# Optimization experiments

Measured on AMD Instinct MI355X. Metric: run time of the kernel, lower is better.

## Reference

```python
import jax, jax.numpy as jnp
import numpy as np

B, N, D = 1, 4301, 768          # batch, tokens (4200 patch + 1 cls + 100 det), dim
H, HD = 12, 64                  # heads, head_dim (all_head_dim = 768)
NDET = 100                      # det tokens at the end of the sequence
EPS = 1e-5                      # torch LayerNorm default eps
SCALE = HD ** -0.5


def setup_inputs() -> dict:
    key = jax.random.key(0)
    ks = jax.random.split(key, 10)
    w = lambda k: jax.random.normal(k, (D, D), dtype=jnp.float32) * 0.02
    return {
        "x": jax.random.normal(ks[0], (B, N, D), dtype=jnp.float32),
        "wq_p": w(ks[1]), "wk_p": w(ks[2]), "wv_p": w(ks[3]),
        "wq_d": w(ks[4]), "wk_d": w(ks[5]), "wv_d": w(ks[6]),
        "bq_p": jnp.zeros((D,), jnp.float32), "bv_p": jnp.zeros((D,), jnp.float32),
        "bq_d": jnp.zeros((D,), jnp.float32), "bv_d": jnp.zeros((D,), jnp.float32),
        "ln_g": jnp.ones((D,), jnp.float32), "ln_b": jnp.zeros((D,), jnp.float32),
        "wo_p": w(ks[7]), "bo_p": jnp.zeros((D,), jnp.float32),
        "wo_d": w(ks[8]), "bo_d": jnp.zeros((D,), jnp.float32),
    }


def reference(x, wq_p, wk_p, wv_p, wq_d, wk_d, wv_d,
              bq_p, bv_p, bq_d, bv_d, ln_g, ln_b,
              wo_p, bo_p, wo_d, bo_d):
    xp = x[:, :-NDET, :]                       # [B, N-100, D] patch (+cls) tokens
    xd = x[:, -NDET:, :]                       # [B, 100, D]   det tokens
    # separate patch/det QKV projections (subln=True path; k has no bias)
    q = jnp.concatenate([xp @ wq_p.T + bq_p, xd @ wq_d.T + bq_d], axis=1)
    k = jnp.concatenate([xp @ wk_p.T,        xd @ wk_d.T],        axis=1)
    v = jnp.concatenate([xp @ wv_p.T + bv_p, xd @ wv_d.T + bv_d], axis=1)
    split = lambda t: t.reshape(B, N, H, HD).transpose(0, 2, 1, 3)  # [B,H,N,HD]
    q, k, v = split(q) * SCALE, split(k), split(v)
    # unfused attention (memory_efficient_attention_pytorch, attn_mask=None)
    attn = jax.nn.softmax(jnp.einsum("bhqd,bhkd->bhqk", q, k), axis=-1)
    o = jnp.einsum("bhqk,bhkd->bhqd", attn, v)
    o = o.transpose(0, 2, 1, 3).reshape(B, N, D)
    # inner_attn_ln (LayerNorm over all_head_dim)
    mu = o.mean(-1, keepdims=True)
    var = ((o - mu) ** 2).mean(-1, keepdims=True)
    o = (o - mu) * jax.lax.rsqrt(var + EPS) * ln_g + ln_b
    # separate patch/det output projections
    out = jnp.concatenate([o[:, :-NDET, :] @ wo_p.T + bo_p,
                           o[:, -NDET:, :] @ wo_d.T + bo_d], axis=1)
    return out
```

## Files before the change

### kernel.cpp

```cpp
#include <hip/hip_runtime.h>
#include <hip/hip_bf16.h>

#define NT 4301
#define NP 4201
#define NDET 100
#define DMODEL 768
#define NHEAD 12
#define HD 64
#define LN_EPS 1e-5f
#define LOG2E 1.4426950408889634f
#define QSCALE (0.125f * LOG2E)
#define NTP 4352
#define NCHUNK 68
#define FRAGSZ 512
#define CHUNKSZ 4096

typedef __hip_bfloat16 bf16;
typedef __attribute__((ext_vector_type(4))) float f32x4;
typedef __attribute__((ext_vector_type(8))) short frag8;

__global__ __launch_bounds__(256) void cast_all_kernel(
    const float* __restrict__ x,
    const float* __restrict__ w0, const float* __restrict__ w1,
    const float* __restrict__ w2, const float* __restrict__ w3,
    const float* __restrict__ w4, const float* __restrict__ w5,
    const float* __restrict__ w6, const float* __restrict__ w7,
    bf16* __restrict__ dst, int nx, int nw, int total) {
    int i4 = (blockIdx.x * 256 + threadIdx.x) * 4;
    if (i4 >= total) return;
    const float* s;
    int off;
    if (i4 < nx) {
        s = x; off = i4;
    } else {
        int r = i4 - nx;
        int w = r / nw;
        off = r - w * nw;
        s = w0;
        if (w == 1) s = w1; else if (w == 2) s = w2; else if (w == 3) s = w3;
        else if (w == 4) s = w4; else if (w == 5) s = w5;
        else if (w == 6) s = w6; else if (w == 7) s = w7;
    }
    float4 v = *(const float4*)(s + off);
    bf16 o[4] = {__float2bfloat16(v.x), __float2bfloat16(v.y),
                 __float2bfloat16(v.z), __float2bfloat16(v.w)};
    *(ushort4*)(dst + i4) = *(ushort4*)o;
}

__global__ __launch_bounds__(256, 4) void qkv_kernel(
    const bf16* __restrict__ xb, const bf16* __restrict__ wbase,
    const float* __restrict__ bq_p, const float* __restrict__ bq_d,
    const float* __restrict__ bv_p, const float* __restrict__ bv_d,
    bf16* __restrict__ Qb, bf16* __restrict__ Ksw, bf16* __restrict__ Vsw) {
    __shared__ bf16 As[64][32];
    __shared__ bf16 Bs[192][32];

    const int tid = threadIdx.x;
    const int wave = tid >> 6, lane = tid & 63;
    const int quad = lane >> 4, l16 = lane & 15;
    const int bx = blockIdx.x;
    const int h = blockIdx.y;
    const int is_det = bx >= 66;
    const int row0 = is_det ? NP + (bx - 66) * 64 : bx * 64;
    const int Mlim = is_det ? NT : NP;
    const int col0 = h * 64;
    const size_t nw = (size_t)DMODEL * DMODEL;
    const bf16* W = wbase + (is_det ? 3 * nw : 0);

    const f32x4 z4 = {0.f, 0.f, 0.f, 0.f};
    f32x4 acc[4][3];
#pragma unroll
    for (int r4 = 0; r4 < 4; ++r4)
#pragma unroll
        for (int f = 0; f < 3; ++f) acc[r4][f] = z4;

    const int srow = tid >> 2;
    const int scol8 = (tid & 3) * 8;
    int a_r = row0 + srow;
    if (a_r >= Mlim) a_r = Mlim - 1;
    const bf16* ap = xb + (size_t)a_r * DMODEL + scol8;
    const bf16* bp = W + (size_t)(col0 + srow) * DMODEL + scol8;

    uint4 areg  = *(const uint4*)(ap);
    uint4 breg0 = *(const uint4*)(bp);
    uint4 breg1 = *(const uint4*)(bp + nw);
    uint4 breg2 = *(const uint4*)(bp + 2 * nw);

    for (int k0 = 0; k0 < DMODEL; k0 += 32) {
        __syncthreads();
        *(uint4*)(&As[srow][scol8]) = areg;
        *(uint4*)(&Bs[srow][scol8]) = breg0;
        *(uint4*)(&Bs[64 + srow][scol8]) = breg1;
        *(uint4*)(&Bs[128 + srow][scol8]) = breg2;
        if (k0 + 32 < DMODEL) {
            areg  = *(const uint4*)(ap + k0 + 32);
            breg0 = *(const uint4*)(bp + k0 + 32);
            breg1 = *(const uint4*)(bp + nw + k0 + 32);
            breg2 = *(const uint4*)(bp + 2 * nw + k0 + 32);
        }
        __asm__ volatile("s_waitcnt lgkmcnt(0)" ::: "memory");
        __builtin_amdgcn_s_barrier();
        __asm__ volatile("" ::: "memory");
        frag8 af[4], bfr[3];
#pragma unroll
        for (int r4 = 0; r4 < 4; ++r4)
            af[r4] = *(const frag8*)(&As[r4 * 16 + l16][quad * 8]);
#pragma unroll
        for (int f = 0; f < 3; ++f)
            bfr[f] = *(const frag8*)(&Bs[wave * 48 + f * 16 + l16][quad * 8]);
#pragma unroll
        for (int r4 = 0; r4 < 4; ++r4)
#pragma unroll
            for (int f = 0; f < 3; ++f)
                acc[r4][f] = __builtin_amdgcn_mfma_f32_16x16x32_bf16(af[r4], bfr[f], acc[r4][f], 0, 0, 0);
        __asm__ volatile("" ::: "memory");
    }

#pragma unroll
    for (int f = 0; f < 3; ++f) {
        const int oc = 3 * wave + f;
        const int opi = oc >> 2;
        const int cin = (oc & 3) * 16 + l16;
        const int c = col0 + cin;
        float bv = 0.f, scale = 1.f;
        if (opi == 0) { bv = (is_det ? bq_d : bq_p)[c]; scale = QSCALE; }
        else if (opi == 2) { bv = (is_det ? bv_d : bv_p)[c]; }
#pragma unroll
        for (int r4 = 0; r4 < 4; ++r4) {
#pragma unroll
            for (int j = 0; j < 4; ++j) {
                const int r = row0 + r4 * 16 + quad * 4 + j;
                if (r >= Mlim) continue;
                const bf16 val = __float2bfloat16((acc[r4][f][j] + bv) * scale);
                if (opi == 0) {
                    Qb[(size_t)r * DMODEL + c] = val;
                } else if (opi == 1) {
                    const int cc = r >> 6, tf = (r >> 4) & 3, ln = r & 15;
                    const int s = cin >> 5, qd = (cin >> 3) & 3, je = cin & 7;
                    Ksw[((size_t)(h * NCHUNK + cc) * 8 + tf * 2 + s) * FRAGSZ +
                        (qd * 16 + ln) * 8 + je] = val;
                } else {
                    const int t = cin >> 4, le = cin & 15;
                    const int cc = r >> 6, rr = r & 63;
                    const int sv = rr >> 5, qv = (rr >> 3) & 3, je = rr & 7;
                    Vsw[((size_t)(h * NCHUNK + cc) * 8 + t * 2 + sv) * FRAGSZ +
                        (qv * 16 + le) * 8 + je] = val;
                }
            }
        }
    }
}

__global__ __launch_bounds__(256, 2) void attn_kernel(
    const bf16* __restrict__ Q, const bf16* __restrict__ Ksw,
    const bf16* __restrict__ Vsw, float* __restrict__ O_part,
    float* __restrict__ l_part, int cpb) {
    __shared__ unsigned short Ps[4][32][72];

    const int tid = threadIdx.x;
    const int wave = tid >> 6, lane = tid & 63;
    const int quad = lane >> 4, l16 = lane & 15;
    const int h = blockIdx.y;
    const int z = blockIdx.z;
    const int qbase = blockIdx.x * 128;
    const int hoff = h * HD;
    const int c0 = z * cpb, c1 = c0 + cpb;

    frag8 ones;
#pragma unroll
    for (int j = 0; j < 8; ++j) ones[j] = (short)0x3F80;

    frag8 qf[2][2];
#pragma unroll
    for (int g = 0; g < 2; ++g) {
        int qr = qbase + wave * 32 + g * 16 + l16;
        if (qr >= NT) qr = NT - 1;
#pragma unroll
        for (int s = 0; s < 2; ++s)
            qf[g][s] = *(const frag8*)(Q + (size_t)qr * DMODEL + hoff + s * 32 + quad * 8);
    }

    const bf16* kb0 = Ksw + (size_t)h * NCHUNK * CHUNKSZ + lane * 8;
    const bf16* vb0 = Vsw + (size_t)h * NCHUNK * CHUNKSZ + lane * 8;

    const f32x4 z4 = {0.f, 0.f, 0.f, 0.f};
    f32x4 accO[2][4], accL[2];
#pragma unroll
    for (int g = 0; g < 2; ++g) {
        accL[g] = z4;
#pragma unroll
        for (int t = 0; t < 4; ++t) accO[g][t] = z4;
    }

    for (int c = c0; c < c1; ++c) {
        const bf16* kc = kb0 + (size_t)c * CHUNKSZ;
        const bf16* vc = vb0 + (size_t)c * CHUNKSZ;
        frag8 kf[8], vf[8];
#pragma unroll
        for (int f = 0; f < 8; ++f) {
            kf[f] = *(const frag8*)(kc + f * FRAGSZ);
            vf[f] = *(const frag8*)(vc + f * FRAGSZ);
        }

        f32x4 S[2][4];
#pragma unroll
        for (int g = 0; g < 2; ++g)
#pragma unroll
            for (int t = 0; t < 4; ++t) {
                f32x4 s0 = __builtin_amdgcn_mfma_f32_16x16x32_bf16(qf[g][0], kf[t * 2 + 0], z4, 0, 0, 0);
                S[g][t]  = __builtin_amdgcn_mfma_f32_16x16x32_bf16(qf[g][1], kf[t * 2 + 1], s0, 0, 0, 0);
            }
        if (c == NCHUNK - 1) {
            const int kbase = c * 64;
#pragma unroll
            for (int t = 0; t < 4; ++t)
                if (kbase + t * 16 + l16 >= NT)
#pragma unroll
                    for (int g = 0; g < 2; ++g)
                        S[g][t][0] = S[g][t][1] = S[g][t][2] = S[g][t][3] = -1e30f;
        }
#pragma unroll
        for (int g = 0; g < 2; ++g)
#pragma unroll
            for (int t = 0; t < 4; ++t)
#pragma unroll
                for (int j = 0; j < 4; j += 2) {
                    float2 f2 = make_float2(__builtin_exp2f(S[g][t][j]),
                                            __builtin_exp2f(S[g][t][j + 1]));
                    __hip_bfloat162 b2 = __float22bfloat162_rn(f2);
                    unsigned int u = *(unsigned int*)&b2;
                    Ps[wave][g * 16 + quad * 4 + j][t * 16 + l16] = (unsigned short)u;
                    Ps[wave][g * 16 + quad * 4 + j + 1][t * 16 + l16] = (unsigned short)(u >> 16);
                }
        __asm__ volatile("" ::: "memory");
#pragma unroll
        for (int s = 0; s < 2; ++s)
#pragma unroll
            for (int g = 0; g < 2; ++g) {
                frag8 pf = *(const frag8*)(&Ps[wave][g * 16 + l16][s * 32 + quad * 8]);
                accL[g] = __builtin_amdgcn_mfma_f32_16x16x32_bf16(pf, ones, accL[g], 0, 0, 0);
#pragma unroll
                for (int t = 0; t < 4; ++t)
                    accO[g][t] = __builtin_amdgcn_mfma_f32_16x16x32_bf16(pf, vf[t * 2 + s], accO[g][t], 0, 0, 0);
            }
        __asm__ volatile("" ::: "memory");
    }

    float* Op = O_part + (size_t)z * NT * DMODEL;
#pragma unroll
    for (int g = 0; g < 2; ++g)
#pragma unroll
        for (int j = 0; j < 4; ++j) {
            const int r = qbase + wave * 32 + g * 16 + quad * 4 + j;
            if (r < NT) {
#pragma unroll
                for (int t = 0; t < 4; ++t)
                    Op[(size_t)r * DMODEL + hoff + t * 16 + l16] = accO[g][t][j];
                if (l16 == 0)
                    l_part[((size_t)z * NHEAD + h) * NTP + r] = accL[g][j];
            }
        }
}

__global__ __launch_bounds__(192) void reduce_ln_kernel(
    const float* __restrict__ O_part, const float* __restrict__ l_part,
    const float* __restrict__ g, const float* __restrict__ b,
    bf16* __restrict__ out, int nsplit) {
    const int n = blockIdx.x;
    const int tid = threadIdx.x;
    const int d0 = tid * 4;
    const int hh = d0 >> 6;

    float4 o = make_float4(0.f, 0.f, 0.f, 0.f);
    float lv = 0.f;
    for (int s = 0; s < nsplit; ++s) {
        float4 v = *(const float4*)(O_part + ((size_t)s * NT + n) * DMODEL + d0);
        o.x += v.x; o.y += v.y; o.z += v.z; o.w += v.w;
        lv += l_part[((size_t)s * NHEAD + hh) * NTP + n];
    }
    const float inv_l = 1.0f / lv;
    float vals[4] = {o.x * inv_l, o.y * inv_l, o.z * inv_l, o.w * inv_l};

    float s = vals[0] + vals[1] + vals[2] + vals[3];
    float s2 = vals[0] * vals[0] + vals[1] * vals[1] + vals[2] * vals[2] + vals[3] * vals[3];
#pragma unroll
    for (int off = 1; off < 64; off <<= 1) {
        s += __shfl_xor(s, off);
        s2 += __shfl_xor(s2, off);
    }
    __shared__ float ss[3], ss2[3];
    const int wave = tid >> 6, lane = tid & 63;
    if (lane == 0) { ss[wave] = s; ss2[wave] = s2; }
    __syncthreads();
    s = ss[0] + ss[1] + ss[2];
    s2 = ss2[0] + ss2[1] + ss2[2];
    const float mu = s * (1.0f / 768.0f);
    float var = s2 * (1.0f / 768.0f) - mu * mu;
    const float inv = rsqrtf(var + LN_EPS);

    unsigned short pk[4];
#pragma unroll
    for (int i = 0; i < 4; ++i) {
        const int d = d0 + i;
        const float v = (vals[i] - mu) * inv * g[d] + b[d];
        bf16 bb = __float2bfloat16(v);
        pk[i] = *(unsigned short*)&bb;
    }
    *(ushort4*)(out + (size_t)n * DMODEL + d0) = *(ushort4*)pk;
}

__global__ __launch_bounds__(256, 2) void out_kernel(
    const bf16* __restrict__ Lb, const bf16* __restrict__ wo,
    const float* __restrict__ bo_p, const float* __restrict__ bo_d,
    float* __restrict__ out) {
    __shared__ bf16 As[128][32];
    __shared__ bf16 Bs[64][32];

    const int tid = threadIdx.x;
    const int wave = tid >> 6, lane = tid & 63;
    const int quad = lane >> 4, l16 = lane & 15;
    const int bx = blockIdx.x;
    const int is_det = bx >= 33;
    const int row0 = is_det ? NP : bx * 128;
    const int Mlim = is_det ? NT : NP;
    const int col0 = blockIdx.y * 64;
    const size_t nw = (size_t)DMODEL * DMODEL;
    const bf16* B = wo + (is_det ? nw : 0);
    const float* bias = is_det ? bo_d : bo_p;

    const f32x4 z4 = {0.f, 0.f, 0.f, 0.f};
    f32x4 acc[2][4];
#pragma unroll
    for (int gg = 0; gg < 2; ++gg)
#pragma unroll
        for (int t = 0; t < 4; ++t) acc[gg][t] = z4;

    const int arow = tid >> 1;
    const int acol = (tid & 1) * 16;
    int a_r = row0 + arow;
    if (a_r >= Mlim) a_r = Mlim - 1;
    const bf16* ap = Lb + (size_t)a_r * DMODEL + acol;
    const int brow = tid >> 2;
    const int bcol = (tid & 3) * 8;
    const bf16* bp = B + (size_t)(col0 + brow) * DMODEL + bcol;

    uint4 areg0 = *(const uint4*)(ap);
    uint4 areg1 = *(const uint4*)(ap + 8);
    uint4 breg  = *(const uint4*)(bp);

    for (int k0 = 0; k0 < DMODEL; k0 += 32) {
        __syncthreads();
        *(uint4*)(&As[arow][acol]) = areg0;
        *(uint4*)(&As[arow][acol + 8]) = areg1;
        *(uint4*)(&Bs[brow][bcol]) = breg;
        if (k0 + 32 < DMODEL) {
            areg0 = *(const uint4*)(ap + k0 + 32);
            areg1 = *(const uint4*)(ap + k0 + 40);
            breg  = *(const uint4*)(bp + k0 + 32);
        }
        __asm__ volatile("s_waitcnt lgkmcnt(0)" ::: "memory");
        __builtin_amdgcn_s_barrier();
        __asm__ volatile("" ::: "memory");
        frag8 af[2], bfq[4];
#pragma unroll
        for (int gg = 0; gg < 2; ++gg)
            af[gg] = *(const frag8*)(&As[wave * 32 + gg * 16 + l16][quad * 8]);
#pragma unroll
        for (int t = 0; t < 4; ++t)
            bfq[t] = *(const frag8*)(&Bs[t * 16 + l16][quad * 8]);
#pragma unroll
        for (int gg = 0; gg < 2; ++gg)
#pragma unroll
            for (int t = 0; t < 4; ++t)
                acc[gg][t] = __builtin_amdgcn_mfma_f32_16x16x32_bf16(af[gg], bfq[t], acc[gg][t], 0, 0, 0);
        __asm__ volatile("" ::: "memory");
    }

#pragma unroll
    for (int gg = 0; gg < 2; ++gg) {
        const int rbase = row0 + wave * 32 + gg * 16 + quad * 4;
#pragma unroll
        for (int t = 0; t < 4; ++t) {
            const int c = col0 + t * 16 + l16;
            const float bv = bias[c];
#pragma unroll
            for (int j = 0; j < 4; ++j) {
                const int r = rbase + j;
                if (r < Mlim) out[(size_t)r * DMODEL + c] = acc[gg][t][j] + bv;
            }
        }
    }
}

extern "C" void kernel_launch(void* const* d_in, const int* in_sizes, int n_in,
                              void* d_out, int out_size, void* d_ws, size_t ws_size,
                              hipStream_t stream) {
    const float* x    = (const float*)d_in[0];
    const float* wq_p = (const float*)d_in[1];
    const float* wk_p = (const float*)d_in[2];
    const float* wv_p = (const float*)d_in[3];
    const float* wq_d = (const float*)d_in[4];
    const float* wk_d = (const float*)d_in[5];
    const float* wv_d = (const float*)d_in[6];
    const float* bq_p = (const float*)d_in[7];
    const float* bv_p = (const float*)d_in[8];
    const float* bq_d = (const float*)d_in[9];
    const float* bv_d = (const float*)d_in[10];
    const float* ln_g = (const float*)d_in[11];
    const float* ln_b = (const float*)d_in[12];
    const float* wo_p = (const float*)d_in[13];
    const float* bo_p = (const float*)d_in[14];
    const float* wo_d = (const float*)d_in[15];
    const float* bo_d = (const float*)d_in[16];
    float* out = (float*)d_out;

    const size_t nx  = (size_t)NT * DMODEL;
    const size_t nsw = (size_t)NHEAD * NCHUNK * CHUNKSZ;
    const size_t nw  = (size_t)DMODEL * DMODEL;

    char* ws = (char*)d_ws;
    bf16* xb   = (bf16*)ws; ws += nx * 2;
    bf16* wqkv = (bf16*)ws; ws += 6 * nw * 2;
    bf16* wob  = (bf16*)ws; ws += 2 * nw * 2;
    bf16* Qb   = (bf16*)ws; ws += nx * 2;
    bf16* Ksw  = (bf16*)ws; ws += nsw * 2;
    bf16* Vsw  = (bf16*)ws; ws += nsw * 2;
    const size_t fixed = (size_t)(ws - (char*)d_ws);

    const size_t per_split = nx * 4 + (size_t)NHEAD * NTP * 4;
    int nsplit = 1;
    if (ws_size >= fixed + 4 * per_split) nsplit = 4;
    else if (ws_size >= fixed + 2 * per_split) nsplit = 2;
    const int cpb = NCHUNK / nsplit;

    float* O_part = (float*)ws;
    float* l_part = (float*)(ws + (size_t)nsplit * nx * 4);
    bf16* Lb = xb;

    const int total = (int)(nx + 8 * nw);
    cast_all_kernel<<<dim3((total / 4 + 255) / 256), dim3(256), 0, stream>>>(
        x, wq_p, wk_p, wv_p, wq_d, wk_d, wv_d, wo_p, wo_d, xb, (int)nx, (int)nw, total);

    qkv_kernel<<<dim3(68, 12), dim3(256), 0, stream>>>(
        xb, wqkv, bq_p, bq_d, bv_p, bv_d, Qb, Ksw, Vsw);

    attn_kernel<<<dim3(34, NHEAD, nsplit), dim3(256), 0, stream>>>(
        Qb, Ksw, Vsw, O_part, l_part, cpb);

    reduce_ln_kernel<<<dim3(NT), dim3(192), 0, stream>>>(
        O_part, l_part, ln_g, ln_b, Lb, nsplit);

    out_kernel<<<dim3(34, 12), dim3(256), 0, stream>>>(Lb, wob, bo_p, bo_d, out);
}
```

Before: 263.6 us.

## Replace LDS round-trip for P fragments with permlane swaps in attention

Computes S transposed (K as the A operand) so each lane holds key-contiguous scores. The bf16 P fragments for the PV MFMA are then assembled in registers with v_permlane32/16_swap instead of being written to and read back from shared memory. This removes the LDS buffer, its stores and loads, and the associated waits per chunk. The tail mask is rewritten for the new per-lane key layout. It relies on the permlane swap instructions and on the register layout matching the MFMA operand layout exactly.

```diff
diff --git a/kernel.cpp b/kernel.cpp
--- a/kernel.cpp
+++ b/kernel.cpp
@@ -18,6 +18,24 @@
 typedef __hip_bfloat16 bf16;
 typedef __attribute__((ext_vector_type(4))) float f32x4;
 typedef __attribute__((ext_vector_type(8))) short frag8;
+typedef __attribute__((ext_vector_type(2))) unsigned int u32x2;
+
+static __device__ __forceinline__ void permlane32_swap(unsigned& a, unsigned& b) {
+#if __has_builtin(__builtin_amdgcn_permlane32_swap)
+    u32x2 r = __builtin_amdgcn_permlane32_swap(a, b, false, false);
+    a = r[0]; b = r[1];
+#else
+    asm("v_permlane32_swap_b32 %0, %1" : "+v"(a), "+v"(b));
+#endif
+}
+static __device__ __forceinline__ void permlane16_swap(unsigned& a, unsigned& b) {
+#if __has_builtin(__builtin_amdgcn_permlane16_swap)
+    u32x2 r = __builtin_amdgcn_permlane16_swap(a, b, false, false);
+    a = r[0]; b = r[1];
+#else
+    asm("v_permlane16_swap_b32 %0, %1" : "+v"(a), "+v"(b));
+#endif
+}
 
 __global__ __launch_bounds__(256) void cast_all_kernel(
     const float* __restrict__ x,
@@ -155,8 +173,6 @@
     const bf16* __restrict__ Q, const bf16* __restrict__ Ksw,
     const bf16* __restrict__ Vsw, float* __restrict__ O_part,
     float* __restrict__ l_part, int cpb) {
-    __shared__ unsigned short Ps[4][32][72];
-
     const int tid = threadIdx.x;
     const int wave = tid >> 6, lane = tid & 63;
     const int quad = lane >> 4, l16 = lane & 15;
@@ -207,43 +223,50 @@
         for (int g = 0; g < 2; ++g)
 #pragma unroll
             for (int t = 0; t < 4; ++t) {
-                f32x4 s0 = __builtin_amdgcn_mfma_f32_16x16x32_bf16(qf[g][0], kf[t * 2 + 0], z4, 0, 0, 0);
-                S[g][t]  = __builtin_amdgcn_mfma_f32_16x16x32_bf16(qf[g][1], kf[t * 2 + 1], s0, 0, 0, 0);
+                f32x4 s0 = __builtin_amdgcn_mfma_f32_16x16x32_bf16(kf[t * 2 + 0], qf[g][0], z4, 0, 0, 0);
+                S[g][t]  = __builtin_amdgcn_mfma_f32_16x16x32_bf16(kf[t * 2 + 1], qf[g][1], s0, 0, 0, 0);
             }
         if (c == NCHUNK - 1) {
-            const int kbase = c * 64;
+            const int kb = c * 64 + quad * 4;
 #pragma unroll
             for (int t = 0; t < 4; ++t)
-                if (kbase + t * 16 + l16 >= NT)
-#pragma unroll
-                    for (int g = 0; g < 2; ++g)
-                        S[g][t][0] = S[g][t][1] = S[g][t][2] = S[g][t][3] = -1e30f;
-        }
-#pragma unroll
-        for (int g = 0; g < 2; ++g)
-#pragma unroll
-            for (int t = 0; t < 4; ++t)
-#pragma unroll
-                for (int j = 0; j < 4; j += 2) {
-                    float2 f2 = make_float2(__builtin_exp2f(S[g][t][j]),
-                                            __builtin_exp2f(S[g][t][j + 1]));
-                    __hip_bfloat162 b2 = __float22bfloat162_rn(f2);
-                    unsigned int u = *(unsigned int*)&b2;
-                    Ps[wave][g * 16 + quad * 4 + j][t * 16 + l16] = (unsigned short)u;
-                    Ps[wave][g * 16 + quad * 4 + j + 1][t * 16 + l16] = (unsigned short)(u >> 16);
-                }
-        __asm__ volatile("" ::: "memory");
-#pragma unroll
-        for (int s = 0; s < 2; ++s)
-#pragma unroll
-            for (int g = 0; g < 2; ++g) {
-                frag8 pf = *(const frag8*)(&Ps[wave][g * 16 + l16][s * 32 + quad * 8]);
+#pragma unroll
+                for (int j = 0; j < 4; ++j)
+                    if (kb + t * 16 + j >= NT) {
+                        S[0][t][j] = -1e30f;
+                        S[1][t][j] = -1e30f;
+                    }
+        }
+
+#pragma unroll
+        for (int g = 0; g < 2; ++g) {
+            unsigned lo[4], hi[4];
+#pragma unroll
+            for (int t = 0; t < 4; ++t) {
+                __hip_bfloat162 b0 = __float22bfloat162_rn(make_float2(
+                    __builtin_exp2f(S[g][t][0]), __builtin_exp2f(S[g][t][1])));
+                __hip_bfloat162 b1 = __float22bfloat162_rn(make_float2(
+                    __builtin_exp2f(S[g][t][2]), __builtin_exp2f(S[g][t][3])));
+                lo[t] = *(unsigned*)&b0;
+                hi[t] = *(unsigned*)&b1;
+            }
+#pragma unroll
+            for (int s = 0; s < 2; ++s) {
+                unsigned A = lo[2 * s], B = hi[2 * s];
+                unsigned C = lo[2 * s + 1], D = hi[2 * s + 1];
+                permlane32_swap(A, C);
+                permlane32_swap(B, D);
+                permlane16_swap(A, C);
+                permlane16_swap(B, D);
+                union { unsigned u[4]; frag8 f; } pu;
+                pu.u[0] = A; pu.u[1] = B; pu.u[2] = C; pu.u[3] = D;
+                const frag8 pf = pu.f;
                 accL[g] = __builtin_amdgcn_mfma_f32_16x16x32_bf16(pf, ones, accL[g], 0, 0, 0);
 #pragma unroll
                 for (int t = 0; t < 4; ++t)
                     accO[g][t] = __builtin_amdgcn_mfma_f32_16x16x32_bf16(pf, vf[t * 2 + s], accO[g][t], 0, 0, 0);
             }
-        __asm__ volatile("" ::: "memory");
+        }
     }
 
     float* Op = O_part + (size_t)z * NT * DMODEL;
```

Result: no change. 265.1 us (+0.6%).
